# Optimization experiments

Measured on AMD Instinct MI355X. Metric: run time of the kernel, lower is better.

The kernel has to match this reference:

```python
import jax, jax.numpy as jnp
import numpy as np

N_DOCS = 500_000
VOCAB = 30522
Q_NNZ = 32
TOP_K = 10


def setup_inputs() -> dict:
    rng = np.random.default_rng(0)
    # irregular row lengths (avg ~128 terms per doc, SPLADE-style)
    lengths = rng.integers(64, 193, size=N_DOCS)
    crow = np.zeros(N_DOCS + 1, dtype=np.int64)
    crow[1:] = np.cumsum(lengths)
    nnz = int(crow[-1])
    indice = jnp.asarray(rng.integers(0, VOCAB, size=nnz).astype(np.int32))
    values = jnp.asarray(rng.random(nnz, dtype=np.float32))

    key = jax.random.key(0)
    k1, k2 = jax.random.split(key)
    q_indices = jax.random.randint(k1, (1, Q_NNZ), 0, VOCAB, dtype=jnp.int32)
    q_values = jax.random.uniform(k2, (1, Q_NNZ), dtype=jnp.float32)
    return {
        "q_indices": q_indices,
        "q_values": q_values,
        "crow": jnp.asarray(crow),
        "indice": indice,
        "values": values,
        "top_k": TOP_K,
    }


def reference(q_indices, q_values, crow, indice, values, top_k):
    n_docs = crow.shape[0] - 1
    nnz = indice.shape[0]
    # sparse COO -> dense query vector (duplicates coalesced by summation,
    # matching torch.sparse_coo_tensor(...).to_dense())
    query = jnp.zeros((VOCAB,), dtype=values.dtype).at[q_indices[0]].add(q_values[0])
    # CSR SpMV: map each nnz to its row via searchsorted on crow, then segment-sum
    row_ids = jnp.searchsorted(crow, jnp.arange(nnz, dtype=crow.dtype), side="right") - 1
    scores = jax.ops.segment_sum(values * query[indice], row_ids, num_segments=n_docs)
    # torch.topk returns (values, indices)
    return jax.lax.top_k(scores, top_k)
```

## Files before the change

### kernel.cpp

```cpp
#include <hip/hip_runtime.h>
#include <cstdint>
#include <cfloat>


#define BM_WORDS 954
#define TOPK     10
#define S1_BLOCKS 256
#define QCAP     64

__device__ __forceinline__ void score_hit(
    int id, int j, const uint32_t* bm, const int* s_qi, const float* s_qv,
    int qn, const int* __restrict__ crow, const float* __restrict__ values,
    int n_docs, float* __restrict__ scores)
{
    if ((bm[id >> 5] >> (id & 31)) & 1u) {
        float qv = 0.f;
        for (int q = 0; q < qn; ++q)
            if (s_qi[q] == id) qv += s_qv[q];
        const float prod = values[j] * qv;
        int lo = 0, hi = n_docs + 1;
        while (lo < hi) {
            const int mid = (lo + hi) >> 1;
            if (crow[mid] <= j) lo = mid + 1; else hi = mid;
        }
        atomicAdd(&scores[lo - 1], prod);
    }
}

__global__ __launch_bounds__(256) void score_kernel(
    const int* __restrict__ q_idx, const float* __restrict__ q_val, int qn,
    const int* __restrict__ crow, const int* __restrict__ indice,
    const float* __restrict__ values, int nnz, int n_docs,
    float* __restrict__ scores)
{
    __shared__ uint32_t bm[BM_WORDS];
    __shared__ int   s_qi[QCAP];
    __shared__ float s_qv[QCAP];

    if (qn > QCAP) qn = QCAP;
    for (int i = threadIdx.x; i < BM_WORDS; i += blockDim.x) bm[i] = 0u;
    __syncthreads();
    for (int i = threadIdx.x; i < qn; i += blockDim.x) {
        const int qi = q_idx[i];
        s_qi[i] = qi;
        s_qv[i] = q_val[i];
        atomicOr(&bm[qi >> 5], 1u << (qi & 31));
    }
    __syncthreads();

    const int nnz4 = nnz >> 2;
    const int gtid = blockIdx.x * blockDim.x + threadIdx.x;
    const int gstride = gridDim.x * blockDim.x;
    const int4* __restrict__ ind4 = (const int4*)indice;

    for (int t = gtid; t < nnz4; t += gstride) {
        const int4 v = ind4[t];
        score_hit(v.x, t * 4 + 0, bm, s_qi, s_qv, qn, crow, values, n_docs, scores);
        score_hit(v.y, t * 4 + 1, bm, s_qi, s_qv, qn, crow, values, n_docs, scores);
        score_hit(v.z, t * 4 + 2, bm, s_qi, s_qv, qn, crow, values, n_docs, scores);
        score_hit(v.w, t * 4 + 3, bm, s_qi, s_qv, qn, crow, values, n_docs, scores);
    }
    if (gtid < (nnz & 3)) {
        const int j = (nnz & ~3) + gtid;
        score_hit(indice[j], j, bm, s_qi, s_qv, qn, crow, values, n_docs, scores);
    }
}

template <bool FINAL>
__global__ __launch_bounds__(64) void topk_kernel(
    const float* __restrict__ vals, const int* __restrict__ ids, int n,
    float* __restrict__ out_v, int* __restrict__ out_i)
{
    const int lane = threadIdx.x;
    float bv[TOPK];
    int   bi[TOPK];
    #pragma unroll
    for (int s = 0; s < TOPK; ++s) { bv[s] = -FLT_MAX; bi[s] = 0x7fffffff; }
    float vmin = -FLT_MAX;
    int   minslot = 0;

    const int start  = blockIdx.x * 64 + lane;
    const int stride = gridDim.x * 64;
    for (int i = start; i < n; i += stride) {
        const float v = vals[i];
        if (v > vmin) {
            bv[minslot] = v;
            bi[minslot] = ids ? ids[i] : i;
            vmin = bv[0]; minslot = 0;
            #pragma unroll
            for (int s = 1; s < TOPK; ++s)
                if (bv[s] < vmin) { vmin = bv[s]; minslot = s; }
        }
    }

    for (int r = 0; r < TOPK; ++r) {
        float lv = bv[0]; int ls = 0;
        #pragma unroll
        for (int s = 1; s < TOPK; ++s)
            if (bv[s] > lv || (bv[s] == lv && bi[s] < bi[ls])) { lv = bv[s]; ls = s; }
        float rv = lv; int rd = bi[ls]; int rl = lane;
        #pragma unroll
        for (int off = 32; off > 0; off >>= 1) {
            const float ov = __shfl_xor(rv, off);
            const int   od = __shfl_xor(rd, off);
            const int   ol = __shfl_xor(rl, off);
            if (ov > rv || (ov == rv && (od < rd || (od == rd && ol < rl)))) {
                rv = ov; rd = od; rl = ol;
            }
        }
        if (lane == rl) { bv[ls] = -FLT_MAX; bi[ls] = 0x7fffffff; }
        if (lane == 0) {
            if (FINAL) {
                out_v[r]        = rv;
                out_v[TOPK + r] = (float)rd;
            } else {
                out_v[blockIdx.x * TOPK + r] = rv;
                out_i[blockIdx.x * TOPK + r] = rd;
            }
        }
    }
}

extern "C" void kernel_launch(void* const* d_in, const int* in_sizes, int n_in,
                              void* d_out, int out_size, void* d_ws, size_t ws_size,
                              hipStream_t stream) {
    const int*   q_idx  = (const int*)  d_in[0];
    const float* q_val  = (const float*)d_in[1];
    const int*   crow   = (const int*)  d_in[2];
    const int*   indice = (const int*)  d_in[3];
    const float* values = (const float*)d_in[4];
    const int qn     = in_sizes[0];
    const int n_docs = in_sizes[2] - 1;
    const int nnz    = in_sizes[3];

    char* ws = (char*)d_ws;
    float* scores = (float*)ws;
    size_t off = ((size_t)n_docs * sizeof(float) + 255) & ~(size_t)255;
    float* candv = (float*)(ws + off);
    int*   candi = (int*)(ws + off + S1_BLOCKS * TOPK * sizeof(float));

    hipMemsetAsync(scores, 0, (size_t)n_docs * sizeof(float), stream);

    score_kernel<<<2048, 256, 0, stream>>>(q_idx, q_val, qn, crow, indice,
                                           values, nnz, n_docs, scores);

    topk_kernel<false><<<S1_BLOCKS, 64, 0, stream>>>(scores, nullptr, n_docs,
                                                     candv, candi);
    topk_kernel<true><<<1, 64, 0, stream>>>(candv, candi, S1_BLOCKS * TOPK,
                                            (float*)d_out, nullptr);
}
```

Measured before the change: 623.7 us.

## Score documents per wavefront instead of per-nnz binary search with atomics

Replaces the flat nnz-parallel scoring, which did a binary search over crow and a global atomicAdd for every query hit, with a row-parallel CSR kernel. Each wavefront handles one document at a time, prefetches the next row bounds, and reduces with wave shuffles before writing the score directly. This removes the memset, the per-hit searches and the atomics. The cost is uneven work across documents and loads of indice that are no longer vectorized int4.

```diff
diff --git a/kernel.cpp b/kernel.cpp
--- a/kernel.cpp
+++ b/kernel.cpp
@@ -7,30 +7,12 @@
 #define TOPK     10
 #define S1_BLOCKS 256
 #define QCAP     64
+#define SCORE_BLOCKS 2048
 
-__device__ __forceinline__ void score_hit(
-    int id, int j, const uint32_t* bm, const int* s_qi, const float* s_qv,
-    int qn, const int* __restrict__ crow, const float* __restrict__ values,
-    int n_docs, float* __restrict__ scores)
-{
-    if ((bm[id >> 5] >> (id & 31)) & 1u) {
-        float qv = 0.f;
-        for (int q = 0; q < qn; ++q)
-            if (s_qi[q] == id) qv += s_qv[q];
-        const float prod = values[j] * qv;
-        int lo = 0, hi = n_docs + 1;
-        while (lo < hi) {
-            const int mid = (lo + hi) >> 1;
-            if (crow[mid] <= j) lo = mid + 1; else hi = mid;
-        }
-        atomicAdd(&scores[lo - 1], prod);
-    }
-}
-
-__global__ __launch_bounds__(256) void score_kernel(
+__global__ __launch_bounds__(256) void score_docs_kernel(
     const int* __restrict__ q_idx, const float* __restrict__ q_val, int qn,
     const int* __restrict__ crow, const int* __restrict__ indice,
-    const float* __restrict__ values, int nnz, int n_docs,
+    const float* __restrict__ values, int n_docs, int docs_per_block,
     float* __restrict__ scores)
 {
     __shared__ uint32_t bm[BM_WORDS];
@@ -38,31 +20,68 @@
     __shared__ float s_qv[QCAP];
 
     if (qn > QCAP) qn = QCAP;
-    for (int i = threadIdx.x; i < BM_WORDS; i += blockDim.x) bm[i] = 0u;
+    for (int i = threadIdx.x; i < BM_WORDS; i += 256) bm[i] = 0u;
     __syncthreads();
-    for (int i = threadIdx.x; i < qn; i += blockDim.x) {
-        const int qi = q_idx[i];
-        s_qi[i] = qi;
-        s_qv[i] = q_val[i];
+    if (threadIdx.x < qn) {
+        const int qi = q_idx[threadIdx.x];
+        s_qi[threadIdx.x] = qi;
+        s_qv[threadIdx.x] = q_val[threadIdx.x];
         atomicOr(&bm[qi >> 5], 1u << (qi & 31));
     }
     __syncthreads();
 
-    const int nnz4 = nnz >> 2;
-    const int gtid = blockIdx.x * blockDim.x + threadIdx.x;
-    const int gstride = gridDim.x * blockDim.x;
-    const int4* __restrict__ ind4 = (const int4*)indice;
+    const int wave = threadIdx.x >> 6;
+    const int lane = threadIdx.x & 63;
+    const int d0 = blockIdx.x * docs_per_block;
+    const int d1 = min(d0 + docs_per_block, n_docs);
 
-    for (int t = gtid; t < nnz4; t += gstride) {
-        const int4 v = ind4[t];
-        score_hit(v.x, t * 4 + 0, bm, s_qi, s_qv, qn, crow, values, n_docs, scores);
-        score_hit(v.y, t * 4 + 1, bm, s_qi, s_qv, qn, crow, values, n_docs, scores);
-        score_hit(v.z, t * 4 + 2, bm, s_qi, s_qv, qn, crow, values, n_docs, scores);
-        score_hit(v.w, t * 4 + 3, bm, s_qi, s_qv, qn, crow, values, n_docs, scores);
-    }
-    if (gtid < (nnz & 3)) {
-        const int j = (nnz & ~3) + gtid;
-        score_hit(indice[j], j, bm, s_qi, s_qv, qn, crow, values, n_docs, scores);
+    int d = d0 + wave;
+    int s = 0, e = 0;
+    if (d < d1) { s = crow[d]; e = crow[d + 1]; }
+
+    while (d < d1) {
+        const int dn = d + 4;
+        int sn = 0, en = 0;
+        if (dn < d1) { sn = crow[dn]; en = crow[dn + 1]; }
+
+        float acc = 0.f;
+        const int len = e - s;
+        if (len <= 192) {
+            const int j0 = s + lane, j1 = j0 + 64, j2 = j1 + 64;
+            const bool m0 = j0 < e, m1 = j1 < e, m2 = j2 < e;
+            const int id0 = m0 ? indice[j0] : 0;
+            const int id1 = m1 ? indice[j1] : 0;
+            const int id2 = m2 ? indice[j2] : 0;
+            if (m0 && ((bm[id0 >> 5] >> (id0 & 31)) & 1u)) {
+                float qv = 0.f;
+                for (int q = 0; q < qn; ++q) if (s_qi[q] == id0) qv += s_qv[q];
+                acc += values[j0] * qv;
+            }
+            if (m1 && ((bm[id1 >> 5] >> (id1 & 31)) & 1u)) {
+                float qv = 0.f;
+                for (int q = 0; q < qn; ++q) if (s_qi[q] == id1) qv += s_qv[q];
+                acc += values[j1] * qv;
+            }
+            if (m2 && ((bm[id2 >> 5] >> (id2 & 31)) & 1u)) {
+                float qv = 0.f;
+                for (int q = 0; q < qn; ++q) if (s_qi[q] == id2) qv += s_qv[q];
+                acc += values[j2] * qv;
+            }
+        } else {
+            for (int j = s + lane; j < e; j += 64) {
+                const int id = indice[j];
+                if ((bm[id >> 5] >> (id & 31)) & 1u) {
+                    float qv = 0.f;
+                    for (int q = 0; q < qn; ++q) if (s_qi[q] == id) qv += s_qv[q];
+                    acc += values[j] * qv;
+                }
+            }
+        }
+        #pragma unroll
+        for (int off = 32; off; off >>= 1) acc += __shfl_xor(acc, off);
+        if (lane == 0) scores[d] = acc;
+
+        d = dn; s = sn; e = en;
     }
 }
 
@@ -131,7 +150,6 @@
     const float* values = (const float*)d_in[4];
     const int qn     = in_sizes[0];
     const int n_docs = in_sizes[2] - 1;
-    const int nnz    = in_sizes[3];
 
     char* ws = (char*)d_ws;
     float* scores = (float*)ws;
@@ -139,10 +157,9 @@
     float* candv = (float*)(ws + off);
     int*   candi = (int*)(ws + off + S1_BLOCKS * TOPK * sizeof(float));
 
-    hipMemsetAsync(scores, 0, (size_t)n_docs * sizeof(float), stream);
-
-    score_kernel<<<2048, 256, 0, stream>>>(q_idx, q_val, qn, crow, indice,
-                                           values, nnz, n_docs, scores);
+    const int docs_per_block = (n_docs + SCORE_BLOCKS - 1) / SCORE_BLOCKS;
+    score_docs_kernel<<<SCORE_BLOCKS, 256, 0, stream>>>(
+        q_idx, q_val, qn, crow, indice, values, n_docs, docs_per_block, scores);
 
     topk_kernel<false><<<S1_BLOCKS, 64, 0, stream>>>(scores, nullptr, n_docs,
                                                      candv, candi);
```

New measurement: 606.8 us. 1.03x faster.
